# Kernel tuning notes

Measured on AMD Instinct MI355X. Metric: run time of the kernel, lower is better.

The kernel has to match this reference:

```python
import math
import jax, jax.numpy as jnp
import numpy as np

SCALE = 1.0
OFFSET = 0.0
B, D, R = 524288, 64, 256


def setup_inputs() -> dict:
    key = jax.random.key(0)
    k1, k2, k3 = jax.random.split(key, 3)
    y = jax.random.uniform(k1, (B, 1), dtype=jnp.float32)  # in [0,1)
    x = jax.random.normal(k2, (B, D), dtype=jnp.float32)
    W = jax.random.normal(k3, (D, R), dtype=jnp.float32) * 0.05
    b = jnp.zeros((R,), dtype=jnp.float32)
    logdet = jnp.zeros((B,), dtype=jnp.float32)
    base_points = jnp.linspace(0.0, 1.0, R, dtype=jnp.float32)
    return {"y": y, "x": x, "W": W, "b": b, "logdet": logdet, "base_points": base_points}


def reference(y, x, W, b, logdet, base_points):
    # f(x): linear layer -> [B, R] logits; softmax + cumsum gives monotone CDF-like features
    basefeatures = jnp.cumsum(jax.nn.softmax(x @ W + b, axis=1), axis=1)  # [B, R]
    # bucketize: number of boundaries <= y, minus 1  == searchsorted(side='right') - 1
    start = jnp.searchsorted(base_points, y[:, 0], side="right") - 1  # [B] in [0, R-2]
    i = jnp.arange(basefeatures.shape[0])
    x0 = base_points[start][:, None]            # [B,1]
    x1 = base_points[start + 1][:, None]        # [B,1]
    f0 = basefeatures[i, start][:, None]        # [B,1]
    f1 = basefeatures[i, start + 1][:, None]    # [B,1]
    slope = (f1 - f0) / (x1 - x0)               # [B,1]
    z = SCALE * (f0 + slope * (y - x0)) + OFFSET
    dlogdet = math.log(SCALE) + jnp.log(jnp.abs(slope[:, 0]))
    return z, x, logdet + dlogdet
```

## Files before the change

kernel.cpp:

```cpp
#include <hip/hip_runtime.h>
#include <hip/hip_bf16.h>


#define NB 524288
#define NWT (NB / 16)

typedef __attribute__((ext_vector_type(4))) float f32x4;
typedef __attribute__((ext_vector_type(8))) __bf16 bf16x8;

#define LOG2E 1.4426950408889634f

static __device__ __forceinline__ unsigned short f2b(float f) {
    unsigned u = __builtin_bit_cast(unsigned, f);
    u += 0x7fffu + ((u >> 16) & 1u);
    return (unsigned short)(u >> 16);
}
static __device__ __forceinline__ unsigned pk2t(float a, float b) {
    return (__builtin_bit_cast(unsigned, a) >> 16) | (__builtin_bit_cast(unsigned, b) & 0xffff0000u);
}

__global__ __launch_bounds__(512, 2) void interp1d_kernel(
    const float* __restrict__ y, const float* __restrict__ x,
    const float* __restrict__ W, const float* __restrict__ bias,
    const float* __restrict__ logdet, const float* __restrict__ bp,
    float* __restrict__ out)
{
    __shared__ unsigned short sW[2 * 16 * 64 * 8];
    __shared__ unsigned short sX[8 * 16 * 72];
    __shared__ float sBP[256];
    __shared__ float sBias[256];

    const int t = threadIdx.x;

    if (t < 256) {
        sBP[t]   = bp[t];
        sBias[t] = bias[t] * LOG2E;
    }
    {
        const int col = t & 255;
        const int k0  = (t >> 8) << 5;
        const int lane16lo = col & 15;
        const int n = col >> 4;
        for (int kk = 0; kk < 32; ++kk) {
            int k = k0 + kk;
            float wv = W[k * 256 + col] * LOG2E;
            int lane16 = ((k >> 3) & 3) * 16 + lane16lo;
            int kb = k >> 5, i = k & 7;
            sW[((kb * 16 + n) * 64 + lane16) * 8 + i] = f2b(wv);
        }
    }
    __syncthreads();

    const int lane = t & 63;
    const int colb = lane & 15;
    const int kH   = lane >> 4;
    unsigned short* myX = &sX[(t >> 6) * (16 * 72)];
    const int nw   = gridDim.x << 3;

    int wt = (blockIdx.x << 3) | (t >> 6);

    f32x4 v0 = {}, v1 = {}, v2 = {}, v3 = {};
    float yv = 0.f, ldv = 0.f;
    if (wt < NWT) {
        const f32x4* xg = reinterpret_cast<const f32x4*>(x) + (size_t)wt * 256;
        v0 = xg[lane]; v1 = xg[64 + lane]; v2 = xg[128 + lane]; v3 = xg[192 + lane];
        yv  = y[(wt << 4) + colb];
        ldv = logdet[(wt << 4) + colb];
    }

    for (; wt < NWT; wt += nw) {
        const int m0 = wt << 4;
        const int wtn = wt + nw;

        f32x4 n0 = {}, n1 = {}, n2 = {}, n3 = {};
        float yn = 0.f, ldn = 0.f;
        if (wtn < NWT) {
            const f32x4* xg = reinterpret_cast<const f32x4*>(x) + (size_t)wtn * 256;
            n0 = xg[lane]; n1 = xg[64 + lane]; n2 = xg[128 + lane]; n3 = xg[192 + lane];
            yn  = y[(wtn << 4) + colb];
            ldn = logdet[(wtn << 4) + colb];
        }

        asm volatile("" ::: "memory");

        f32x4* xo = reinterpret_cast<f32x4*>(out + NB) + (size_t)wt * 256;
        __builtin_nontemporal_store(v0, xo + lane);
        __builtin_nontemporal_store(v1, xo + 64 + lane);
        __builtin_nontemporal_store(v2, xo + 128 + lane);
        __builtin_nontemporal_store(v3, xo + 192 + lane);

        {
            uint2 w; int c, row, pos;
            c = lane;        row = c >> 4; pos = c & 15;
            w.x = pk2t(v0[0], v0[1]); w.y = pk2t(v0[2], v0[3]);
            *reinterpret_cast<uint2*>(&myX[row * 72 + pos * 4]) = w;
            c = 64 + lane;   row = c >> 4; pos = c & 15;
            w.x = pk2t(v1[0], v1[1]); w.y = pk2t(v1[2], v1[3]);
            *reinterpret_cast<uint2*>(&myX[row * 72 + pos * 4]) = w;
            c = 128 + lane;  row = c >> 4; pos = c & 15;
            w.x = pk2t(v2[0], v2[1]); w.y = pk2t(v2[2], v2[3]);
            *reinterpret_cast<uint2*>(&myX[row * 72 + pos * 4]) = w;
            c = 192 + lane;  row = c >> 4; pos = c & 15;
            w.x = pk2t(v3[0], v3[1]); w.y = pk2t(v3[2], v3[3]);
            *reinterpret_cast<uint2*>(&myX[row * 72 + pos * 4]) = w;
        }

        bf16x8 a0 = *reinterpret_cast<const bf16x8*>(&myX[colb * 72 + (kH << 3)]);
        bf16x8 a1 = *reinterpret_cast<const bf16x8*>(&myX[colb * 72 + 32 + (kH << 3)]);

        int s = (int)floorf(yv * 255.0f);
        s = min(254, max(0, s));
        s += (sBP[s + 1] <= yv) ? 1 : 0;
        s = min(s, 254);
        s -= (sBP[s] > yv) ? 1 : 0;
        s = max(s, 0);

        const int sb  = s >> 4,  so  = s & 15;
        const int sb1 = (s + 1) >> 4, so1 = (s + 1) & 15;
        float m[4], pm[4];
        #pragma unroll
        for (int j = 0; j < 4; ++j) {
            m[j]  = ((kH << 2) + j <= so)  ? 1.f : 0.f;
            pm[j] = ((kH << 2) + j == so1) ? 1.f : 0.f;
        }

        float denom = 0.f, f0s = 0.f, p1 = 0.f;
        #pragma unroll
        for (int n = 0; n < 16; ++n) {
            bf16x8 w0 = *reinterpret_cast<const bf16x8*>(&sW[(n * 64 + lane) * 8]);
            bf16x8 w1 = *reinterpret_cast<const bf16x8*>(&sW[((16 + n) * 64 + lane) * 8]);
            f32x4 c = *reinterpret_cast<const f32x4*>(&sBias[(n << 4) + (kH << 2)]);
            c = __builtin_amdgcn_mfma_f32_16x16x32_bf16(w0, a0, c, 0, 0, 0);
            c = __builtin_amdgcn_mfma_f32_16x16x32_bf16(w1, a1, c, 0, 0, 0);
            float e0 = __builtin_amdgcn_exp2f(c[0]);
            float e1 = __builtin_amdgcn_exp2f(c[1]);
            float e2 = __builtin_amdgcn_exp2f(c[2]);
            float e3 = __builtin_amdgcn_exp2f(c[3]);
            float bs = (e0 + e1) + (e2 + e3);
            denom += bs;
            float t0 = fmaf(e3, m[3], fmaf(e2, m[2], fmaf(e1, m[1], e0 * m[0])));
            float tp = fmaf(e3, pm[3], fmaf(e2, pm[2], fmaf(e1, pm[1], e0 * pm[0])));
            f0s += (n < sb) ? bs : ((n == sb) ? t0 : 0.f);
            p1  += (n == sb1) ? tp : 0.f;
        }

        denom += __shfl_xor(denom, 16, 64);
        f0s   += __shfl_xor(f0s,   16, 64);
        p1    += __shfl_xor(p1,    16, 64);
        denom += __shfl_xor(denom, 32, 64);
        f0s   += __shfl_xor(f0s,   32, 64);
        p1    += __shfl_xor(p1,    32, 64);

        if (kH == 0) {
            float x0 = sBP[s], x1 = sBP[s + 1];
            float inv = 1.0f / denom;
            float f0 = f0s * inv;
            float slope = (p1 * inv) / (x1 - x0);
            __builtin_nontemporal_store(fmaf(slope, yv - x0, f0), out + m0 + colb);
            __builtin_nontemporal_store(ldv + __logf(fabsf(slope)),
                                        out + (size_t)NB * 65 + m0 + colb);
        }

        if (wtn < NWT) {
            v0 = n0; v1 = n1; v2 = n2; v3 = n3;
            yv = yn; ldv = ldn;
        }
    }
}

extern "C" void kernel_launch(void* const* d_in, const int* in_sizes, int n_in,
                              void* d_out, int out_size, void* d_ws, size_t ws_size,
                              hipStream_t stream) {
    (void)in_sizes; (void)n_in; (void)out_size; (void)d_ws; (void)ws_size;
    const float* y      = (const float*)d_in[0];
    const float* x      = (const float*)d_in[1];
    const float* W      = (const float*)d_in[2];
    const float* b      = (const float*)d_in[3];
    const float* logdet = (const float*)d_in[4];
    const float* bp     = (const float*)d_in[5];
    float* out = (float*)d_out;
    interp1d_kernel<<<dim3(1024), dim3(512), 0, stream>>>(y, x, W, b, logdet, bp, out);
}
```

Baseline: 56.04 us.

## Fully unroll four tiles per wave with two-deep load prefetch

Replaces the grid-stride loop, which prefetched one tile ahead, with a fixed four-tile sequence per wave. Each wave issues global loads two tiles ahead of the tile it is processing, so more memory requests are in flight. This relies on NWT equalling exactly four times the wave count, which holds for the hardcoded grid of 1024 blocks of 8 waves, and drops the bounds checks. The extra tile buffers raise register pressure.

```diff
diff --git a/kernel.cpp b/kernel.cpp
--- a/kernel.cpp
+++ b/kernel.cpp
@@ -17,6 +17,106 @@
 }
 static __device__ __forceinline__ unsigned pk2t(float a, float b) {
     return (__builtin_bit_cast(unsigned, a) >> 16) | (__builtin_bit_cast(unsigned, b) & 0xffff0000u);
+}
+
+struct Tile { f32x4 v0, v1, v2, v3; float yv, ldv; };
+
+static __device__ __forceinline__ void loadT(
+    Tile& T, int wt, int lane, int colb,
+    const float* __restrict__ x, const float* __restrict__ y,
+    const float* __restrict__ logdet)
+{
+    const f32x4* xg = reinterpret_cast<const f32x4*>(x) + (size_t)wt * 256;
+    T.v0 = xg[lane]; T.v1 = xg[64 + lane]; T.v2 = xg[128 + lane]; T.v3 = xg[192 + lane];
+    T.yv  = y[(wt << 4) + colb];
+    T.ldv = logdet[(wt << 4) + colb];
+}
+
+static __device__ __forceinline__ void process(
+    const Tile& T, int wt, int lane, int colb, int kH,
+    unsigned short* myX, const unsigned short* sW,
+    const float* sBP, const float* sBias, float* __restrict__ out)
+{
+    const int m0 = wt << 4;
+
+    f32x4* xo = reinterpret_cast<f32x4*>(out + NB) + (size_t)wt * 256;
+    __builtin_nontemporal_store(T.v0, xo + lane);
+    __builtin_nontemporal_store(T.v1, xo + 64 + lane);
+    __builtin_nontemporal_store(T.v2, xo + 128 + lane);
+    __builtin_nontemporal_store(T.v3, xo + 192 + lane);
+
+    {
+        uint2 w; int c, row, pos;
+        c = lane;        row = c >> 4; pos = c & 15;
+        w.x = pk2t(T.v0[0], T.v0[1]); w.y = pk2t(T.v0[2], T.v0[3]);
+        *reinterpret_cast<uint2*>(&myX[row * 72 + pos * 4]) = w;
+        c = 64 + lane;   row = c >> 4; pos = c & 15;
+        w.x = pk2t(T.v1[0], T.v1[1]); w.y = pk2t(T.v1[2], T.v1[3]);
+        *reinterpret_cast<uint2*>(&myX[row * 72 + pos * 4]) = w;
+        c = 128 + lane;  row = c >> 4; pos = c & 15;
+        w.x = pk2t(T.v2[0], T.v2[1]); w.y = pk2t(T.v2[2], T.v2[3]);
+        *reinterpret_cast<uint2*>(&myX[row * 72 + pos * 4]) = w;
+        c = 192 + lane;  row = c >> 4; pos = c & 15;
+        w.x = pk2t(T.v3[0], T.v3[1]); w.y = pk2t(T.v3[2], T.v3[3]);
+        *reinterpret_cast<uint2*>(&myX[row * 72 + pos * 4]) = w;
+    }
+
+    bf16x8 a0 = *reinterpret_cast<const bf16x8*>(&myX[colb * 72 + (kH << 3)]);
+    bf16x8 a1 = *reinterpret_cast<const bf16x8*>(&myX[colb * 72 + 32 + (kH << 3)]);
+
+    float yv = T.yv;
+    int s = (int)floorf(yv * 255.0f);
+    s = min(254, max(0, s));
+    s += (sBP[s + 1] <= yv) ? 1 : 0;
+    s = min(s, 254);
+    s -= (sBP[s] > yv) ? 1 : 0;
+    s = max(s, 0);
+
+    const int sb  = s >> 4,  so  = s & 15;
+    const int sb1 = (s + 1) >> 4, so1 = (s + 1) & 15;
+    float m[4], pm[4];
+    #pragma unroll
+    for (int j = 0; j < 4; ++j) {
+        m[j]  = ((kH << 2) + j <= so)  ? 1.f : 0.f;
+        pm[j] = ((kH << 2) + j == so1) ? 1.f : 0.f;
+    }
+
+    float denom = 0.f, f0s = 0.f, p1 = 0.f;
+    #pragma unroll
+    for (int n = 0; n < 16; ++n) {
+        bf16x8 w0 = *reinterpret_cast<const bf16x8*>(&sW[(n * 64 + lane) * 8]);
+        bf16x8 w1 = *reinterpret_cast<const bf16x8*>(&sW[((16 + n) * 64 + lane) * 8]);
+        f32x4 c = *reinterpret_cast<const f32x4*>(&sBias[(n << 4) + (kH << 2)]);
+        c = __builtin_amdgcn_mfma_f32_16x16x32_bf16(w0, a0, c, 0, 0, 0);
+        c = __builtin_amdgcn_mfma_f32_16x16x32_bf16(w1, a1, c, 0, 0, 0);
+        float e0 = __builtin_amdgcn_exp2f(c[0]);
+        float e1 = __builtin_amdgcn_exp2f(c[1]);
+        float e2 = __builtin_amdgcn_exp2f(c[2]);
+        float e3 = __builtin_amdgcn_exp2f(c[3]);
+        float bs = (e0 + e1) + (e2 + e3);
+        denom += bs;
+        float t0 = fmaf(e3, m[3], fmaf(e2, m[2], fmaf(e1, m[1], e0 * m[0])));
+        float tp = fmaf(e3, pm[3], fmaf(e2, pm[2], fmaf(e1, pm[1], e0 * pm[0])));
+        f0s += (n < sb) ? bs : ((n == sb) ? t0 : 0.f);
+        p1  += (n == sb1) ? tp : 0.f;
+    }
+
+    denom += __shfl_xor(denom, 16, 64);
+    f0s   += __shfl_xor(f0s,   16, 64);
+    p1    += __shfl_xor(p1,    16, 64);
+    denom += __shfl_xor(denom, 32, 64);
+    f0s   += __shfl_xor(f0s,   32, 64);
+    p1    += __shfl_xor(p1,    32, 64);
+
+    if (kH == 0) {
+        float x0 = sBP[s], x1 = sBP[s + 1];
+        float inv = 1.0f / denom;
+        float f0 = f0s * inv;
+        float slope = (p1 * inv) / (x1 - x0);
+        __builtin_nontemporal_store(fmaf(slope, yv - x0, f0), out + m0 + colb);
+        __builtin_nontemporal_store(T.ldv + __logf(fabsf(slope)),
+                                    out + (size_t)NB * 65 + m0 + colb);
+    }
 }
 
 __global__ __launch_bounds__(512, 2) void interp1d_kernel(
@@ -55,117 +155,26 @@
     const int colb = lane & 15;
     const int kH   = lane >> 4;
     unsigned short* myX = &sX[(t >> 6) * (16 * 72)];
-    const int nw   = gridDim.x << 3;
+    const int nw = gridDim.x << 3;
+    const int wt0 = (blockIdx.x << 3) | (t >> 6);
 
-    int wt = (blockIdx.x << 3) | (t >> 6);
+    Tile T0, T1, T2, T3;
+    loadT(T0, wt0,          lane, colb, x, y, logdet);
+    loadT(T1, wt0 + nw,     lane, colb, x, y, logdet);
 
-    f32x4 v0 = {}, v1 = {}, v2 = {}, v3 = {};
-    float yv = 0.f, ldv = 0.f;
-    if (wt < NWT) {
-        const f32x4* xg = reinterpret_cast<const f32x4*>(x) + (size_t)wt * 256;
-        v0 = xg[lane]; v1 = xg[64 + lane]; v2 = xg[128 + lane]; v3 = xg[192 + lane];
-        yv  = y[(wt << 4) + colb];
-        ldv = logdet[(wt << 4) + colb];
-    }
+    asm volatile("" ::: "memory");
+    loadT(T2, wt0 + 2 * nw, lane, colb, x, y, logdet);
+    process(T0, wt0,          lane, colb, kH, myX, sW, sBP, sBias, out);
 
-    for (; wt < NWT; wt += nw) {
-        const int m0 = wt << 4;
-        const int wtn = wt + nw;
+    asm volatile("" ::: "memory");
+    loadT(T3, wt0 + 3 * nw, lane, colb, x, y, logdet);
+    process(T1, wt0 + nw,     lane, colb, kH, myX, sW, sBP, sBias, out);
 
-        f32x4 n0 = {}, n1 = {}, n2 = {}, n3 = {};
-        float yn = 0.f, ldn = 0.f;
-        if (wtn < NWT) {
-            const f32x4* xg = reinterpret_cast<const f32x4*>(x) + (size_t)wtn * 256;
-            n0 = xg[lane]; n1 = xg[64 + lane]; n2 = xg[128 + lane]; n3 = xg[192 + lane];
-            yn  = y[(wtn << 4) + colb];
-            ldn = logdet[(wtn << 4) + colb];
-        }
+    asm volatile("" ::: "memory");
+    process(T2, wt0 + 2 * nw, lane, colb, kH, myX, sW, sBP, sBias, out);
 
-        asm volatile("" ::: "memory");
-
-        f32x4* xo = reinterpret_cast<f32x4*>(out + NB) + (size_t)wt * 256;
-        __builtin_nontemporal_store(v0, xo + lane);
-        __builtin_nontemporal_store(v1, xo + 64 + lane);
-        __builtin_nontemporal_store(v2, xo + 128 + lane);
-        __builtin_nontemporal_store(v3, xo + 192 + lane);
-
-        {
-            uint2 w; int c, row, pos;
-            c = lane;        row = c >> 4; pos = c & 15;
-            w.x = pk2t(v0[0], v0[1]); w.y = pk2t(v0[2], v0[3]);
-            *reinterpret_cast<uint2*>(&myX[row * 72 + pos * 4]) = w;
-            c = 64 + lane;   row = c >> 4; pos = c & 15;
-            w.x = pk2t(v1[0], v1[1]); w.y = pk2t(v1[2], v1[3]);
-            *reinterpret_cast<uint2*>(&myX[row * 72 + pos * 4]) = w;
-            c = 128 + lane;  row = c >> 4; pos = c & 15;
-            w.x = pk2t(v2[0], v2[1]); w.y = pk2t(v2[2], v2[3]);
-            *reinterpret_cast<uint2*>(&myX[row * 72 + pos * 4]) = w;
-            c = 192 + lane;  row = c >> 4; pos = c & 15;
-            w.x = pk2t(v3[0], v3[1]); w.y = pk2t(v3[2], v3[3]);
-            *reinterpret_cast<uint2*>(&myX[row * 72 + pos * 4]) = w;
-        }
-
-        bf16x8 a0 = *reinterpret_cast<const bf16x8*>(&myX[colb * 72 + (kH << 3)]);
-        bf16x8 a1 = *reinterpret_cast<const bf16x8*>(&myX[colb * 72 + 32 + (kH << 3)]);
-
-        int s = (int)floorf(yv * 255.0f);
-        s = min(254, max(0, s));
-        s += (sBP[s + 1] <= yv) ? 1 : 0;
-        s = min(s, 254);
-        s -= (sBP[s] > yv) ? 1 : 0;
-        s = max(s, 0);
-
-        const int sb  = s >> 4,  so  = s & 15;
-        const int sb1 = (s + 1) >> 4, so1 = (s + 1) & 15;
-        float m[4], pm[4];
-        #pragma unroll
-        for (int j = 0; j < 4; ++j) {
-            m[j]  = ((kH << 2) + j <= so)  ? 1.f : 0.f;
-            pm[j] = ((kH << 2) + j == so1) ? 1.f : 0.f;
-        }
-
-        float denom = 0.f, f0s = 0.f, p1 = 0.f;
-        #pragma unroll
-        for (int n = 0; n < 16; ++n) {
-            bf16x8 w0 = *reinterpret_cast<const bf16x8*>(&sW[(n * 64 + lane) * 8]);
-            bf16x8 w1 = *reinterpret_cast<const bf16x8*>(&sW[((16 + n) * 64 + lane) * 8]);
-            f32x4 c = *reinterpret_cast<const f32x4*>(&sBias[(n << 4) + (kH << 2)]);
-            c = __builtin_amdgcn_mfma_f32_16x16x32_bf16(w0, a0, c, 0, 0, 0);
-            c = __builtin_amdgcn_mfma_f32_16x16x32_bf16(w1, a1, c, 0, 0, 0);
-            float e0 = __builtin_amdgcn_exp2f(c[0]);
-            float e1 = __builtin_amdgcn_exp2f(c[1]);
-            float e2 = __builtin_amdgcn_exp2f(c[2]);
-            float e3 = __builtin_amdgcn_exp2f(c[3]);
-            float bs = (e0 + e1) + (e2 + e3);
-            denom += bs;
-            float t0 = fmaf(e3, m[3], fmaf(e2, m[2], fmaf(e1, m[1], e0 * m[0])));
-            float tp = fmaf(e3, pm[3], fmaf(e2, pm[2], fmaf(e1, pm[1], e0 * pm[0])));
-            f0s += (n < sb) ? bs : ((n == sb) ? t0 : 0.f);
-            p1  += (n == sb1) ? tp : 0.f;
-        }
-
-        denom += __shfl_xor(denom, 16, 64);
-        f0s   += __shfl_xor(f0s,   16, 64);
-        p1    += __shfl_xor(p1,    16, 64);
-        denom += __shfl_xor(denom, 32, 64);
-        f0s   += __shfl_xor(f0s,   32, 64);
-        p1    += __shfl_xor(p1,    32, 64);
-
-        if (kH == 0) {
-            float x0 = sBP[s], x1 = sBP[s + 1];
-            float inv = 1.0f / denom;
-            float f0 = f0s * inv;
-            float slope = (p1 * inv) / (x1 - x0);
-            __builtin_nontemporal_store(fmaf(slope, yv - x0, f0), out + m0 + colb);
-            __builtin_nontemporal_store(ldv + __logf(fabsf(slope)),
-                                        out + (size_t)NB * 65 + m0 + colb);
-        }
-
-        if (wtn < NWT) {
-            v0 = n0; v1 = n1; v2 = n2; v3 = n3;
-            yv = yn; ldv = ldn;
-        }
-    }
+    asm volatile("" ::: "memory");
+    process(T3, wt0 + 3 * nw, lane, colb, kH, myX, sW, sBP, sBias, out);
 }
 
 extern "C" void kernel_launch(void* const* d_in, const int* in_sizes, int n_in,
```

Result: no change. 55.30 us (-1.3%).
